# Performance work log

Measured on AMD Instinct MI355X. Metric: run time of the kernel, lower is better.

Reference implementation:

```python
import jax, jax.numpy as jnp
import numpy as np

N = 1024
DIM = 128
HEADS = 8
DK = DIM // HEADS
EDIM = 16
EPS = 1e-5
NEG = -10000.0


def _lin(k, din, dout):
    return jax.random.normal(k, (din, dout), jnp.float32) * (1.0 / np.sqrt(din))


def setup_inputs() -> dict:
    key = jax.random.key(0)
    ks = jax.random.split(key, 10)
    mask = jax.random.randint(ks[2], (N, N), 0, 2).astype(bool)
    mask = mask | jnp.eye(N, dtype=bool)  # self-loops always valid
    return {
        "x": jax.random.normal(ks[0], (N, DIM), jnp.float32),
        "edge_feat": jax.random.normal(ks[1], (N, N, EDIM), jnp.float32),
        "mask": mask,
        "Wq": _lin(ks[3], DIM, DIM), "bq": jnp.zeros((DIM,), jnp.float32),
        "Wk": _lin(ks[4], DIM, DIM), "bk": jnp.zeros((DIM,), jnp.float32),
        "Wv": _lin(ks[5], DIM, DIM), "bv": jnp.zeros((DIM,), jnp.float32),
        "Wae": _lin(ks[6], EDIM, HEADS), "bae": jnp.zeros((HEADS,), jnp.float32),
        "Wve": _lin(ks[7], EDIM, DIM), "bve": jnp.zeros((DIM,), jnp.float32),
        "Wo": _lin(ks[8], DIM, DIM), "bo": jnp.zeros((DIM,), jnp.float32),
        "gamma": jnp.ones((DIM,), jnp.float32),
        "beta": jnp.zeros((DIM,), jnp.float32),
    }


def reference(x, edge_feat, mask, Wq, bq, Wk, bk, Wv, bv, Wae, bae, Wve, bve, Wo, bo, gamma, beta):
    n, dim = x.shape
    heads = bae.shape[0]
    dk = dim // heads
    # pre-LayerNorm
    mu = jnp.mean(x, axis=-1, keepdims=True)
    var = jnp.mean(jnp.square(x - mu), axis=-1, keepdims=True)
    h = (x - mu) * jax.lax.rsqrt(var + EPS) * gamma + beta
    q = (h @ Wq + bq).reshape(n, heads, dk)
    k = (h @ Wk + bk).reshape(n, heads, dk)
    v = (h @ Wv + bv).reshape(n, heads, dk)
    # attention logits with per-edge additive bias: (n, m, heads)
    att = jnp.einsum('nhd,mhd->nmh', q, k) / np.sqrt(dk).astype(np.float32)
    att = att + edge_feat @ Wae + bae
    att = jnp.where(mask[..., None], att, NEG)
    alpha = jax.nn.softmax(att, axis=1)  # softmax over source nodes m
    # edge-conditioned values: msg_{nm} = v_m + U(e_{nm})
    edge_val = (edge_feat @ Wve + bve).reshape(n, n, heads, dk)
    out = jnp.einsum('nmh,mhd->nhd', alpha, v) + jnp.einsum('nmh,nmhd->nhd', alpha, edge_val)
    out = out.reshape(n, dim) @ Wo + bo
    return x + out
```

## Files before the change

kernel.cpp:

```cpp
#include <hip/hip_runtime.h>
#include <hip/hip_bf16.h>

#define NNODE 1024
#define DIM 128
#define HEADS 8
#define DK 16
#define EDIM 16
#define BN 8
#define NGRP 8
#define LOG2E 1.44269504f

#define PAR 768
#define WREG (2 * PAR)
#define SMEM_F 8448

__global__ __launch_bounds__(384)
void ln_qkv_kernel(const float* __restrict__ x,
                   const float* __restrict__ Wq, const float* __restrict__ bq,
                   const float* __restrict__ Wk, const float* __restrict__ bk,
                   const float* __restrict__ Wv, const float* __restrict__ bv,
                   const float* __restrict__ gamma, const float* __restrict__ beta,
                   const int* __restrict__ mask,
                   float* __restrict__ qg, float* __restrict__ kg, float* __restrict__ vg,
                   unsigned char* __restrict__ maskb) {
    const int n = blockIdx.x;
    const int t = threadIdx.x;
    __shared__ float hrow[DIM];
    __shared__ float part[4];

    if (t < 128) {
        const int* mrow = mask + (size_t)n * NNODE + t * 8;
        unsigned pb = 0;
        #pragma unroll
        for (int i = 0; i < 8; ++i) pb |= (mrow[i] ? 1u : 0u) << i;
        maskb[(size_t)n * 128 + t] = (unsigned char)pb;
    }

    float xv = 0.f;
    if (t < 128) {
        xv = x[n * DIM + t];
        float v = xv;
        #pragma unroll
        for (int off = 32; off >= 1; off >>= 1) v += __shfl_xor(v, off);
        if ((t & 63) == 0) part[t >> 6] = v;
    }
    __syncthreads();
    const float mu = (part[0] + part[1]) * (1.0f / DIM);
    const float dx = xv - mu;
    if (t < 128) {
        float v = dx * dx;
        #pragma unroll
        for (int off = 32; off >= 1; off >>= 1) v += __shfl_xor(v, off);
        if ((t & 63) == 0) part[2 + (t >> 6)] = v;
    }
    __syncthreads();
    if (t < 128) {
        const float var = (part[2] + part[3]) * (1.0f / DIM);
        hrow[t] = dx * rsqrtf(var + 1e-5f) * gamma[t] + beta[t];
    }
    __syncthreads();

    const int which = t >> 7;
    const int col = t & 127;
    const float* W = (which == 0) ? Wq : (which == 1) ? Wk : Wv;
    const float* b = (which == 0) ? bq : (which == 1) ? bk : bv;
    float* o       = (which == 0) ? qg : (which == 1) ? kg : vg;
    float a0 = b[col], a1 = 0.f;
    #pragma unroll 8
    for (int i = 0; i < DIM; i += 2) {
        a0 = fmaf(hrow[i],     W[i * DIM + col],       a0);
        a1 = fmaf(hrow[i + 1], W[(i + 1) * DIM + col], a1);
    }
    o[n * DIM + col] = a0 + a1;
}

__device__ __forceinline__ void gll16(const float* g, float* l) {
    auto* gp = (const __attribute__((address_space(1))) unsigned int*)(g);
    auto* lp = (__attribute__((address_space(3))) unsigned int*)(l);
    __builtin_amdgcn_global_load_lds(gp, lp, 16, 0, 0);
}

__global__ __launch_bounds__(256, 2)
void attn_kernel(const float* __restrict__ qg, const float* __restrict__ kg,
                 const float* __restrict__ vg, const float* __restrict__ ef,
                 const unsigned char* __restrict__ maskb,
                 const float* __restrict__ Wae, const float* __restrict__ bae,
                 float* __restrict__ acc) {
    const int t = threadIdx.x;
    const int lane = t & 63;
    const int wid = t >> 6;
    const int sp = lane >> 5;
    const int np = (lane >> 3) & 3;
    const int h  = lane & 7;
    const int bx = blockIdx.x;
    const int n0  = (bx >> 3) * BN;
    const int grp = bx & 7;
    const int mb_w = grp * 128 + wid * 32;

    __shared__ float smem[SMEM_F];
    float* wreg = smem + wid * WREG;

    float qreg[2][DK];
    #pragma unroll
    for (int hf = 0; hf < 2; ++hf) {
        const float* qp = qg + (size_t)(n0 + np + 4 * hf) * DIM + h * DK;
        #pragma unroll
        for (int d4 = 0; d4 < 4; ++d4) {
            const float4 qv = *(const float4*)(qp + d4 * 4);
            qreg[hf][d4 * 4 + 0] = qv.x; qreg[hf][d4 * 4 + 1] = qv.y;
            qreg[hf][d4 * 4 + 2] = qv.z; qreg[hf][d4 * 4 + 3] = qv.w;
        }
    }
    float waec[EDIM];
    #pragma unroll
    for (int e = 0; e < EDIM; ++e) waec[e] = Wae[e * HEADS + h] * LOG2E;
    const float baeh = bae[h] * LOG2E;

    unsigned mk0 = *(const unsigned*)(maskb + (size_t)(n0 + np)     * 128 + (mb_w >> 3)) >> sp;
    unsigned mk1 = *(const unsigned*)(maskb + (size_t)(n0 + np + 4) * 128 + (mb_w >> 3)) >> sp;

    float sl[2] = {0.f, 0.f};
    float accv[2][DK], accT[2][EDIM];
    #pragma unroll
    for (int hf = 0; hf < 2; ++hf) {
        #pragma unroll
        for (int d = 0; d < DK; ++d) accv[hf][d] = 0.f;
        #pragma unroll
        for (int e = 0; e < EDIM; ++e) accT[hf][e] = 0.f;
    }

    const int s0   = lane & 3;
    const int h0   = (lane >> 2) & 7;
    const int row0 = lane >> 5;
    const int koffl = row0 * 128 + h0 * 16 + (((s0 - (h0 >> 1)) & 3) << 2);
    const int nn0 = lane >> 3;
    const int mm0 = (lane >> 2) & 1;
    const int eoffl = nn0 * (NNODE * EDIM) + mm0 * EDIM + (((s0 - nn0) & 3) << 2);
    const float* efb = ef + (size_t)n0 * NNODE * EDIM;

    int krot[4], erot[4];
    const int rotk = (h >> 1) & 3;
    #pragma unroll
    for (int i = 0; i < 4; ++i) {
        krot[i] = ((i + rotk) & 3) << 2;
        erot[i] = ((i + np) & 3) << 2;
    }

#define ISSUE_BATCH(DB, MB)                                              \
    do {                                                                 \
        float* db = (DB);                                                \
        gll16(kg + (size_t)(MB) * DIM + koffl, db);                      \
        gll16(vg + (size_t)(MB) * DIM + koffl, db + 256);                \
        gll16(efb + (size_t)(MB) * EDIM + eoffl, db + 512);              \
    } while (0)

#define COMPUTE_CHUNK(DB)                                                      \
    do {                                                                       \
        __builtin_amdgcn_s_setprio(1);                                         \
        const float* kl = (DB) + sp * 128 + h * 16;                            \
        const float* vl = kl + 256;                                            \
        const float* eb = (DB) + 512 + np * 32 + sp * 16;                      \
        float kk[DK], vv[DK];                                                  \
        _Pragma("unroll")                                                      \
        for (int i = 0; i < 4; ++i) {                                          \
            const float4 k4 = *(const float4*)(kl + krot[i]);                  \
            kk[i*4+0]=k4.x; kk[i*4+1]=k4.y; kk[i*4+2]=k4.z; kk[i*4+3]=k4.w;    \
            const float4 v4 = *(const float4*)(vl + krot[i]);                  \
            vv[i*4+0]=v4.x; vv[i*4+1]=v4.y; vv[i*4+2]=v4.z; vv[i*4+3]=v4.w;    \
        }                                                                      \
        _Pragma("unroll")                                                      \
        for (int hf = 0; hf < 2; ++hf) {                                       \
            float efv[EDIM];                                                   \
            _Pragma("unroll")                                                  \
            for (int i = 0; i < 4; ++i) {                                      \
                const float4 e4 = *(const float4*)(eb + hf * 128 + erot[i]);   \
                efv[i*4+0]=e4.x; efv[i*4+1]=e4.y;                              \
                efv[i*4+2]=e4.z; efv[i*4+3]=e4.w;                              \
            }                                                                  \
            float bias = baeh, dot = 0.f;                                      \
            _Pragma("unroll")                                                  \
            for (int e = 0; e < EDIM; ++e) bias = fmaf(efv[e], waec[e], bias); \
            _Pragma("unroll")                                                  \
            for (int d = 0; d < DK; ++d) dot = fmaf(qreg[hf][d], kk[d], dot);  \
            const float lg = fmaf(dot, 0.25f * LOG2E, bias);                   \
            const unsigned mv = (hf ? mk1 : mk0) & 1u;                         \
            const float p = mv ? __builtin_amdgcn_exp2f(lg) : 0.f;             \
            sl[hf] += p;                                                       \
            _Pragma("unroll")                                                  \
            for (int d = 0; d < DK; ++d) accv[hf][d] = fmaf(p, vv[d], accv[hf][d]); \
            _Pragma("unroll")                                                  \
            for (int e = 0; e < EDIM; ++e) accT[hf][e] = fmaf(p, efv[e], accT[hf][e]); \
        }                                                                      \
        mk0 >>= 2; mk1 >>= 2;                                                  \
        __builtin_amdgcn_s_setprio(0);                                         \
    } while (0)

    ISSUE_BATCH(wreg, mb_w);

    #pragma unroll 1
    for (int cc = 0; cc < 16; cc += 2) {
        ISSUE_BATCH(wreg + PAR, mb_w + 2 * (cc + 1));
        asm volatile("s_waitcnt vmcnt(3)" ::: "memory");
        COMPUTE_CHUNK(wreg);
        if (cc < 14) {
            ISSUE_BATCH(wreg, mb_w + 2 * (cc + 2));
            asm volatile("s_waitcnt vmcnt(3)" ::: "memory");
        } else {
            asm volatile("s_waitcnt vmcnt(0)" ::: "memory");
        }
        COMPUTE_CHUNK(wreg + PAR);
    }
#undef ISSUE_BATCH
#undef COMPUTE_CHUNK

    #pragma unroll
    for (int hf = 0; hf < 2; ++hf) {
        sl[hf] += __shfl_xor(sl[hf], 32);
        #pragma unroll
        for (int d = 0; d < DK; ++d) accv[hf][d] += __shfl_xor(accv[hf][d], 32);
        #pragma unroll
        for (int e = 0; e < EDIM; ++e) accT[hf][e] += __shfl_xor(accT[hf][e], 32);
    }
    __syncthreads();
    float* red = smem;
    if (lane < 32) {
        float* rp = &red[((wid * 4 + np) * 8 + h) * 66];
        #pragma unroll
        for (int hf = 0; hf < 2; ++hf) {
            rp[hf * 33 + 0] = sl[hf];
            #pragma unroll
            for (int d = 0; d < DK; ++d) rp[hf * 33 + 1 + d] = accv[hf][d];
            #pragma unroll
            for (int e = 0; e < EDIM; ++e) rp[hf * 33 + 17 + e] = accT[hf][e];
        }
    }
    __syncthreads();
    for (int v = t; v < BN * HEADS * 33; v += 256) {
        const int n = v / 264;
        const int rem = v - n * 264;
        const int hh = rem / 33;
        const int idx = rem - hh * 33;
        const int nnp = n & 3, hf = n >> 2;
        float sum = 0.f;
        #pragma unroll
        for (int w = 0; w < 4; ++w)
            sum += red[((w * 4 + nnp) * 8 + hh) * 66 + hf * 33 + idx];
        acc[((size_t)(n0 + n) * NGRP + grp) * 264 + rem] = sum;
    }
}

__global__ __launch_bounds__(128)
void final_kernel(const float* __restrict__ acc,
                  const float* __restrict__ Wve, const float* __restrict__ bve,
                  const float* __restrict__ x,
                  const float* __restrict__ Wo, const float* __restrict__ bo,
                  float* __restrict__ out) {
    const int n = blockIdx.x, t = threadIdx.x;
    __shared__ float ab[HEADS * 33];
    __shared__ float orow[DIM];
    const float* ap = acc + (size_t)n * NGRP * 264;
    for (int u = t; u < HEADS * 33; u += 128) {
        float sv = 0.f;
        #pragma unroll
        for (int g = 0; g < NGRP; ++g) sv += ap[g * 264 + u];
        ab[u] = sv;
    }
    __syncthreads();
    const int col = t, hh = col >> 4, dd = col & 15;
    const float slv = ab[hh * 33];
    float acc2 = 0.f;
    #pragma unroll
    for (int e = 0; e < EDIM; ++e) acc2 = fmaf(ab[hh * 33 + 17 + e], Wve[e * DIM + col], acc2);
    orow[col] = (ab[hh * 33 + 1 + dd] + acc2) / slv + bve[col];
    __syncthreads();
    float o0 = bo[col] + x[(size_t)n * DIM + col], o1 = 0.f;
    #pragma unroll 8
    for (int i = 0; i < DIM; i += 2) {
        o0 = fmaf(orow[i],     Wo[i * DIM + col],       o0);
        o1 = fmaf(orow[i + 1], Wo[(i + 1) * DIM + col], o1);
    }
    out[(size_t)n * DIM + col] = o0 + o1;
}

extern "C" void kernel_launch(void* const* d_in, const int* in_sizes, int n_in,
                              void* d_out, int out_size, void* d_ws, size_t ws_size,
                              hipStream_t stream) {
    const float* x     = (const float*)d_in[0];
    const float* ef    = (const float*)d_in[1];
    const int*   mask  = (const int*)d_in[2];
    const float* Wq    = (const float*)d_in[3];
    const float* bq    = (const float*)d_in[4];
    const float* Wk    = (const float*)d_in[5];
    const float* bk    = (const float*)d_in[6];
    const float* Wv    = (const float*)d_in[7];
    const float* bv    = (const float*)d_in[8];
    const float* Wae   = (const float*)d_in[9];
    const float* bae   = (const float*)d_in[10];
    const float* Wve   = (const float*)d_in[11];
    const float* bve   = (const float*)d_in[12];
    const float* Wo    = (const float*)d_in[13];
    const float* bo    = (const float*)d_in[14];
    const float* gamma = (const float*)d_in[15];
    const float* beta  = (const float*)d_in[16];

    float* ws = (float*)d_ws;
    float* accb = ws;
    float* qg   = ws + (size_t)NNODE * NGRP * 264;
    float* kg   = qg + (size_t)NNODE * DIM;
    float* vg   = kg + (size_t)NNODE * DIM;
    unsigned char* maskb = (unsigned char*)(vg + (size_t)NNODE * DIM);

    ln_qkv_kernel<<<NNODE, 384, 0, stream>>>(x, Wq, bq, Wk, bk, Wv, bv, gamma, beta,
                                             mask, qg, kg, vg, maskb);
    attn_kernel<<<(NNODE / BN) * NGRP, 256, 0, stream>>>(qg, kg, vg, ef, maskb, Wae, bae, accb);
    final_kernel<<<NNODE, 128, 0, stream>>>(accb, Wve, bve, x, Wo, bo, (float*)d_out);
}
```

Baseline: 163.7 us.

## Prefetch edge features two chunks ahead with separate quad-buffered region

Splits the per-chunk loads into K/V batches (double-buffered) and edge-feature loads (quad-buffered in their own LDS region). Edge features, the dominant HBM stream, are issued two chunks ahead while K/V stay one chunk ahead, which deepens the prefetch on the bandwidth-heavy stream. The price is more LDS per wave (WREG grows) and more complex vmcnt accounting, which could lower occupancy or introduce ordering hazards.

```diff
diff --git a/kernel.cpp b/kernel.cpp
--- a/kernel.cpp
+++ b/kernel.cpp
@@ -10,8 +10,7 @@
 #define NGRP 8
 #define LOG2E 1.44269504f
 
-#define PAR 768
-#define WREG (2 * PAR)
+#define WREG 2048
 #define SMEM_F 8448
 
 __global__ __launch_bounds__(384)
@@ -146,20 +145,23 @@
         erot[i] = ((i + np) & 3) << 2;
     }
 
-#define ISSUE_BATCH(DB, MB)                                              \
+#define KVB(p) (wreg + (p) * 512)
+
+#define ISSUE_KV(DB, MB)                                                 \
     do {                                                                 \
-        float* db = (DB);                                                \
-        gll16(kg + (size_t)(MB) * DIM + koffl, db);                      \
-        gll16(vg + (size_t)(MB) * DIM + koffl, db + 256);                \
-        gll16(efb + (size_t)(MB) * EDIM + eoffl, db + 512);              \
+        gll16(kg + (size_t)(MB) * DIM + koffl, (DB));                    \
+        gll16(vg + (size_t)(MB) * DIM + koffl, (DB) + 256);              \
     } while (0)
 
-#define COMPUTE_CHUNK(DB)                                                      \
+#define ISSUE_EF(EOFF, MB)                                               \
+    gll16(efb + (size_t)(MB) * EDIM + eoffl, wreg + 1024 + (EOFF))
+
+#define COMPUTE_CHUNK(DB, EB)                                                  \
     do {                                                                       \
         __builtin_amdgcn_s_setprio(1);                                         \
         const float* kl = (DB) + sp * 128 + h * 16;                            \
         const float* vl = kl + 256;                                            \
-        const float* eb = (DB) + 512 + np * 32 + sp * 16;                      \
+        const float* eb = (EB) + np * 32 + sp * 16;                            \
         float kk[DK], vv[DK];                                                  \
         _Pragma("unroll")                                                      \
         for (int i = 0; i < 4; ++i) {                                          \
@@ -195,23 +197,32 @@
         __builtin_amdgcn_s_setprio(0);                                         \
     } while (0)
 
-    ISSUE_BATCH(wreg, mb_w);
+    ISSUE_EF(0, mb_w);
+    ISSUE_KV(KVB(0), mb_w);
+    ISSUE_EF(256, mb_w + 2);
+    int eoff = 0;
 
     #pragma unroll 1
-    for (int cc = 0; cc < 16; cc += 2) {
-        ISSUE_BATCH(wreg + PAR, mb_w + 2 * (cc + 1));
-        asm volatile("s_waitcnt vmcnt(3)" ::: "memory");
-        COMPUTE_CHUNK(wreg);
-        if (cc < 14) {
-            ISSUE_BATCH(wreg, mb_w + 2 * (cc + 2));
-            asm volatile("s_waitcnt vmcnt(3)" ::: "memory");
-        } else {
-            asm volatile("s_waitcnt vmcnt(0)" ::: "memory");
-        }
-        COMPUTE_CHUNK(wreg + PAR);
-    }
-#undef ISSUE_BATCH
+    for (int cc = 0; cc < 14; cc += 2) {
+        ISSUE_KV(KVB(1), mb_w + 2 * (cc + 1));
+        ISSUE_EF(eoff ^ 512, mb_w + 2 * (cc + 2));
+        asm volatile("s_waitcnt vmcnt(4)" ::: "memory");
+        COMPUTE_CHUNK(KVB(0), wreg + 1024 + eoff);
+        ISSUE_KV(KVB(0), mb_w + 2 * (cc + 2));
+        ISSUE_EF((eoff ^ 512) + 256, mb_w + 2 * (cc + 3));
+        asm volatile("s_waitcnt vmcnt(4)" ::: "memory");
+        COMPUTE_CHUNK(KVB(1), wreg + 1024 + eoff + 256);
+        eoff ^= 512;
+    }
+    ISSUE_KV(KVB(1), mb_w + 30);
+    asm volatile("s_waitcnt vmcnt(3)" ::: "memory");
+    COMPUTE_CHUNK(KVB(0), wreg + 1024 + eoff);
+    asm volatile("s_waitcnt vmcnt(0)" ::: "memory");
+    COMPUTE_CHUNK(KVB(1), wreg + 1024 + eoff + 256);
+#undef ISSUE_KV
+#undef ISSUE_EF
 #undef COMPUTE_CHUNK
+#undef KVB
 
     #pragma unroll
     for (int hf = 0; hf < 2; ++hf) {
```

After: 172.6 us. +5.5%, slower.
